# Optimization experiments

Measured on AMD Instinct MI355X. Metric: run time of the kernel, lower is better.

Reference implementation:

```python
import jax, jax.numpy as jnp
import numpy as np

N, E, DIM, H = 100000, 1600000, 128, 8
HD = DIM // H  # head_dim


def setup_inputs() -> dict:
    key = jax.random.key(0)
    ks = jax.random.split(key, 12)
    s = lambda k, sh, fan: jax.random.normal(k, sh, jnp.float32) * (1.0 / np.sqrt(fan))
    return {
        "x": jax.random.normal(ks[0], (N, DIM), jnp.float32),
        "src": jax.random.randint(ks[1], (E,), 0, N, jnp.int32),
        "dst": jax.random.randint(ks[2], (E,), 0, N, jnp.int32),
        # input_linear: dim -> dim
        "w_in": s(ks[3], (DIM, DIM), DIM), "b_in": jnp.zeros((DIM,), jnp.float32),
        # attn_linear_u: dim -> H (with bias); attn_linear_v: dim -> H (no bias)
        "w_au": s(ks[4], (DIM, H), DIM), "b_au": jnp.zeros((H,), jnp.float32),
        "w_av": s(ks[5], (DIM, H), DIM),
        # feed-forward: dim -> dim (hidden_dim_multiplier=1) -> dim
        "w1": s(ks[6], (DIM, DIM), DIM), "b1": jnp.zeros((DIM,), jnp.float32),
        "w2": s(ks[7], (DIM, DIM), DIM), "b2": jnpp if False else jnp.zeros((DIM,), jnp.float32),
    }


def reference(x, src, dst, w_in, b_in, w_au, b_au, w_av, w1, b1, w2, b2):
    n = x.shape[0]
    h = x @ w_in + b_in                      # [N, dim]
    a_u = h @ w_au + b_au                    # [N, H]
    a_v = h @ w_av                           # [N, H]
    # u_add_v: per-edge scores, then LeakyReLU(0.2)
    scores = jax.nn.leaky_relu(a_u[src] + a_v[dst], negative_slope=0.2)  # [E, H]
    # edge_softmax: normalize over incoming edges of each dst node
    smax = jax.ops.segment_max(scores, dst, num_segments=n)              # [N, H]
    ex = jnp.exp(scores - smax[dst])                                     # [E, H]
    denom = jax.ops.segment_sum(ex, dst, num_segments=n)                 # [N, H]
    probs = ex / denom[dst]                                              # [E, H]
    # u_mul_e_sum with x reshaped to [N, head_dim, H]
    hv = h.reshape(n, HD, H)
    msg = hv[src] * probs[:, None, :]                                    # [E, HD, H]
    agg = jax.ops.segment_sum(msg, dst, num_segments=n)                  # [N, HD, H]
    out = agg.reshape(n, DIM)
    # feed-forward (dropout=0, eval)
    out = jax.nn.gelu(out @ w1 + b1) @ w2 + b2
    return out
```

## Files before the change

kernel.cpp:

```cpp
#include <hip/hip_runtime.h>
#include <hip/hip_bf16.h>
#include <stdint.h>

#define DIM 128
#define NH 8
#define CH 4096
#define BK 128
#define LS 136
#define EBUF 4096

using bf16 = __hip_bfloat16;
typedef __attribute__((ext_vector_type(8))) short short8;
typedef __attribute__((ext_vector_type(4))) float floatx4;


__device__ inline float bf2f(unsigned short b) {
    return __uint_as_float(((unsigned)b) << 16);
}
__device__ inline unsigned short f2bf(float f) {
    unsigned u = __float_as_uint(f);
    u += 0x7FFFu + ((u >> 16) & 1u);
    return (unsigned short)(u >> 16);
}

__device__ inline float gelu_tanh(float x) {
    float x3 = x * x * x;
    float u = 0.7978845608028654f * (x + 0.044715f * x3);
    float e = __expf(2.f * u);
    float t = 1.f - 2.f / (e + 1.f);
    return 0.5f * x * (1.f + t);
}

__launch_bounds__(256)
__global__ void count_pre_kernel(const int* __restrict__ dst, int* __restrict__ mat,
                                 int E, int K, int B,
                                 const float* __restrict__ w_in, const float* __restrict__ w1,
                                 const float* __restrict__ w2, const float* __restrict__ w_au,
                                 const float* __restrict__ w_av,
                                 unsigned short* __restrict__ w_in_b, unsigned short* __restrict__ w1_b,
                                 unsigned short* __restrict__ w2_b, unsigned short* __restrict__ wc_b) {
    __shared__ int cnt[1024];
    const int b = blockIdx.x, tid = threadIdx.x;
    if (b < B) {
        for (int k = tid; k < K; k += 256) cnt[k] = 0;
        __syncthreads();
        const int base = b * CH, end = min(base + CH, E);
        for (int i = base + tid; i < end; i += 256)
            atomicAdd(&cnt[dst[i] >> 7], 1);
        __syncthreads();
        for (int k = tid; k < K; k += 256) mat[(size_t)k * B + b] = cnt[k];
    } else {
        int pb = b - B;
        if (pb < 12) {
            const int m = pb >> 2, qtr = pb & 3;
            const float* W = m == 0 ? w_in : (m == 1 ? w1 : w2);
            unsigned short* O = m == 0 ? w_in_b : (m == 1 ? w1_b : w2_b);
            const bool perm = (m == 1);
            #pragma unroll
            for (int i = 0; i < 16; ++i) {
                int o = qtr * 4096 + tid + i * 256;
                int k = o & 127, n = o >> 7;
                int krow = perm ? ((k & 15) * 8 + (k >> 4)) : k;
                O[o] = f2bf(W[krow * 128 + n]);
            }
        } else {
            #pragma unroll
            for (int i = 0; i < 8; ++i) {
                int o = tid + i * 256;
                int j = o >> 7, kt = o & 127;
                int ko = (kt & 15) * 8 + (kt >> 4);
                float v = (j < 8) ? w_au[ko * 8 + j] : w_av[ko * 8 + (j - 8)];
                wc_b[o] = f2bf(v);
            }
        }
    }
}

__device__ __forceinline__ void stage_pre(unsigned short* wt, const unsigned short* __restrict__ pre,
                                          int tid) {
    #pragma unroll
    for (int i = 0; i < 4; ++i) {
        int g = tid + i * 512;
        short8 v = *(const short8*)(pre + g * 8);
        *(short8*)(wt + (g >> 4) * LS + (g & 15) * 8) = v;
    }
}

__launch_bounds__(512)
__global__ void gemm_in_attn_kernel(const float* __restrict__ x, const unsigned short* __restrict__ w_in_b,
                                    const float* __restrict__ b_in,
                                    const unsigned short* __restrict__ wc_b, const float* __restrict__ b_au,
                                    bf16* __restrict__ h, float* __restrict__ au,
                                    float* __restrict__ av, int M) {
    __shared__ __align__(16) unsigned short wt[128 * LS];
    __shared__ __align__(16) unsigned short wc[16 * LS];
    const int tid = threadIdx.x;

    stage_pre(wt, w_in_b, tid);
    {
        int j = tid >> 5, kt4 = (tid & 31) * 4;
        const unsigned* s = (const unsigned*)(wc_b + j * 128 + kt4);
        unsigned* d = (unsigned*)(wc + j * LS + kt4);
        d[0] = s[0]; d[1] = s[1];
    }
    __syncthreads();

    const int wave = tid >> 6;
    const int lane = tid & 63;
    const int l15 = lane & 15;
    const int q = lane >> 4;
    const int rowbase = blockIdx.x * 128 + wave * 16;
    const int rowA = min(rowbase + l15, M - 1);

    floatx4 acc[8];
    #pragma unroll
    for (int c = 0; c < 8; ++c) acc[c] = (floatx4){0.f, 0.f, 0.f, 0.f};

    #pragma unroll
    for (int kk = 0; kk < 4; ++kk) {
        const float* ap = x + (size_t)rowA * 128 + kk * 32 + q * 8;
        floatx4 a0 = *(const floatx4*)ap;
        floatx4 a1 = *(const floatx4*)(ap + 4);
        union { short8 s; unsigned short u[8]; } cv;
        #pragma unroll
        for (int j = 0; j < 4; ++j) { cv.u[j] = f2bf(a0[j]); cv.u[4 + j] = f2bf(a1[j]); }
        short8 afrag = cv.s;
        #pragma unroll
        for (int c = 0; c < 8; ++c) {
            short8 bfrag = *(const short8*)(wt + (c * 16 + l15) * LS + kk * 32 + q * 8);
            acc[c] = __builtin_amdgcn_mfma_f32_16x16x32_bf16(afrag, bfrag, acc[c], 0, 0, 0);
        }
    }
    __syncthreads();

    const int rl0 = wave * 16 + q * 4;
    #pragma unroll
    for (int c = 0; c < 8; ++c) {
        int col = c * 16 + l15;
        int colw = (col & 7) * 16 + (col >> 3);
        float b = b_in[col];
        #pragma unroll
        for (int r = 0; r < 4; ++r)
            wt[(rl0 + r) * LS + colw] = f2bf(acc[c][r] + b);
    }
    __syncthreads();

    const int blk0 = blockIdx.x * 128;
    #pragma unroll
    for (int i = 0; i < 4; ++i) {
        int g = tid + i * 512;
        int row = g >> 4;
        if (blk0 + row < M) {
            short8 v = *(const short8*)(wt + row * LS + (g & 15) * 8);
            *(short8*)((unsigned short*)h + (size_t)(blk0 + row) * 128 + (g & 15) * 8) = v;
        }
    }

    floatx4 acc2 = (floatx4){0.f, 0.f, 0.f, 0.f};
    #pragma unroll
    for (int kk = 0; kk < 4; ++kk) {
        short8 af = *(const short8*)(wt + (wave * 16 + l15) * LS + kk * 32 + q * 8);
        short8 bf = *(const short8*)(wc + l15 * LS + kk * 32 + q * 8);
        acc2 = __builtin_amdgcn_mfma_f32_16x16x32_bf16(af, bf, acc2, 0, 0, 0);
    }
    {
        const int row0 = rowbase + q * 4;
        int col = l15;
        #pragma unroll
        for (int r = 0; r < 4; ++r) {
            int rr = row0 + r;
            if (rr < M) {
                if (col < 8) au[(size_t)rr * 8 + col] = acc2[r] + b_au[col];
                else         av[(size_t)rr * 8 + (col - 8)] = acc2[r];
            }
        }
    }
}

__launch_bounds__(512)
__global__ void ff_kernel(const bf16* __restrict__ A, const unsigned short* __restrict__ w1_b,
                          const float* __restrict__ b1, const unsigned short* __restrict__ w2_b,
                          const float* __restrict__ b2, float* __restrict__ out, int M) {
    __shared__ __align__(16) unsigned short wt[128 * LS];
    __shared__ __align__(16) unsigned short ht[128 * LS];
    const int tid = threadIdx.x;

    stage_pre(wt, w1_b, tid);
    __syncthreads();

    const int wave = tid >> 6;
    const int lane = tid & 63;
    const int l15 = lane & 15;
    const int q = lane >> 4;
    const int rowbase = blockIdx.x * 128 + wave * 16;
    const int rowA = min(rowbase + l15, M - 1);

    floatx4 acc[8];
    #pragma unroll
    for (int c = 0; c < 8; ++c) acc[c] = (floatx4){0.f, 0.f, 0.f, 0.f};

    #pragma unroll
    for (int kk = 0; kk < 4; ++kk) {
        short8 afrag = *(const short8*)((const unsigned short*)A + (size_t)rowA * 128 + kk * 32 + q * 8);
        #pragma unroll
        for (int c = 0; c < 8; ++c) {
            short8 bfrag = *(const short8*)(wt + (c * 16 + l15) * LS + kk * 32 + q * 8);
            acc[c] = __builtin_amdgcn_mfma_f32_16x16x32_bf16(afrag, bfrag, acc[c], 0, 0, 0);
        }
    }
    __syncthreads();

    stage_pre(wt, w2_b, tid);
    const int rl0 = wave * 16 + q * 4;
    #pragma unroll
    for (int c = 0; c < 8; ++c) {
        int col = c * 16 + l15;
        float b = b1[col];
        #pragma unroll
        for (int r = 0; r < 4; ++r)
            ht[(rl0 + r) * LS + col] = f2bf(gelu_tanh(acc[c][r] + b));
    }
    __syncthreads();

    floatx4 acc2[8];
    #pragma unroll
    for (int c = 0; c < 8; ++c) acc2[c] = (floatx4){0.f, 0.f, 0.f, 0.f};
    #pragma unroll
    for (int kk = 0; kk < 4; ++kk) {
        short8 af = *(const short8*)(ht + (wave * 16 + l15) * LS + kk * 32 + q * 8);
        #pragma unroll
        for (int c = 0; c < 8; ++c) {
            short8 bfrag = *(const short8*)(wt + (c * 16 + l15) * LS + kk * 32 + q * 8);
            acc2[c] = __builtin_amdgcn_mfma_f32_16x16x32_bf16(af, bfrag, acc2[c], 0, 0, 0);
        }
    }

    const int row0 = rowbase + q * 4;
    #pragma unroll
    for (int c = 0; c < 8; ++c) {
        int col = c * 16 + l15;
        float b = b2[col];
        #pragma unroll
        for (int r = 0; r < 4; ++r) {
            int rr = row0 + r;
            if (rr < M) out[(size_t)rr * 128 + col] = acc2[c][r] + b;
        }
    }
}


__launch_bounds__(64)
__global__ void scan_bucket_kernel(int* __restrict__ mat, int* __restrict__ btot, int B) {
    const int k = blockIdx.x;
    const int lane = threadIdx.x;
    const size_t base = (size_t)k * B;
    int carry = 0;
    for (int i0 = 0; i0 < B; i0 += 64) {
        int idx = i0 + lane;
        int v = (idx < B) ? mat[base + idx] : 0;
        int incl = v;
        #pragma unroll
        for (int off = 1; off < 64; off <<= 1) {
            int y = __shfl_up(incl, off);
            if (lane >= off) incl += y;
        }
        int tot = __shfl(incl, 63);
        if (idx < B) mat[base + idx] = carry + incl - v;
        carry += tot;
    }
    if (lane == 0) btot[k] = carry;
}

__launch_bounds__(64)
__global__ void scan_total_kernel(const int* __restrict__ btot, int* __restrict__ bbase, int K) {
    const int lane = threadIdx.x;
    int carry = 0;
    for (int i0 = 0; i0 < K; i0 += 64) {
        int idx = i0 + lane;
        int v = (idx < K) ? btot[idx] : 0;
        int incl = v;
        #pragma unroll
        for (int off = 1; off < 64; off <<= 1) {
            int y = __shfl_up(incl, off);
            if (lane >= off) incl += y;
        }
        int tot = __shfl(incl, 63);
        if (idx < K) bbase[idx] = carry + incl - v;
        carry += tot;
    }
}

__launch_bounds__(256)
__global__ void bucket_scatter_kernel(const int* __restrict__ src, const int* __restrict__ dst,
                                      int* __restrict__ lofs, unsigned* __restrict__ packed,
                                      int E, int K, int B) {
    __shared__ int hist[1024];
    __shared__ int cur[1024];
    __shared__ int wsum[4];
    const int b = blockIdx.x, tid = threadIdx.x;
    for (int k = tid; k < 1024; k += 256) hist[k] = 0;
    __syncthreads();
    const int base = b * CH, end = min(base + CH, E);
    for (int i = base + tid; i < end; i += 256)
        atomicAdd(&hist[dst[i] >> 7], 1);
    __syncthreads();
    int v[4]; int t = 0;
    #pragma unroll
    for (int j = 0; j < 4; ++j) { int x = hist[tid * 4 + j]; v[j] = t; t += x; }
    const int lane = tid & 63, wv = tid >> 6;
    int incl = t;
    #pragma unroll
    for (int off = 1; off < 64; off <<= 1) {
        int y = __shfl_up(incl, off);
        if (lane >= off) incl += y;
    }
    if (lane == 63) wsum[wv] = incl;
    __syncthreads();
    int woff = 0;
    #pragma unroll
    for (int w = 0; w < 4; ++w) if (w < wv) woff += wsum[w];
    int texcl = woff + incl - t;
    #pragma unroll
    for (int j = 0; j < 4; ++j) {
        int k = tid * 4 + j;
        int e = texcl + v[j];
        cur[k] = e;
        if (k < K) lofs[(size_t)b * K + k] = e;
    }
    __syncthreads();
    for (int i = base + tid; i < end; i += 256) {
        int d = dst[i], s = src[i];
        int pos = atomicAdd(&cur[d >> 7], 1);
        packed[(size_t)b * CH + pos] = (unsigned)s | ((unsigned)(d & 127) << 20);
    }
}

__launch_bounds__(256)
__global__ void bucket_csr_kernel(const unsigned* __restrict__ packed, const int* __restrict__ lofs,
                                  const int* __restrict__ mat,
                                  const int* __restrict__ bbase, const int* __restrict__ btot,
                                  int* __restrict__ rowptr, int* __restrict__ deg,
                                  int* __restrict__ esrc, int N, int E, int K, int B) {
    __shared__ unsigned ebuf[EBUF];
    __shared__ int hist[128], cur[128];
    __shared__ int wtot;
    const int k = blockIdx.x, tid = threadIdx.x;
    const int start = bbase[k];
    const int cnt = btot[k];

    for (int b = tid; b < B; b += 256) {
        int lo = lofs[(size_t)b * K + k];
        int chunk_len = min(CH, E - b * CH);
        int hi = (k + 1 < K) ? lofs[(size_t)b * K + k + 1] : chunk_len;
        int dbase = mat[(size_t)k * B + b];
        const unsigned* sp = packed + (size_t)b * CH;
        for (int j = lo; j < hi; ++j) ebuf[dbase + (j - lo)] = sp[j];
    }
    if (tid < 128) hist[tid] = 0;
    __syncthreads();

    for (int i = tid; i < cnt; i += 256)
        atomicAdd(&hist[ebuf[i] >> 20], 1);
    __syncthreads();

    const int lane = tid & 63;
    int v = (tid < 128) ? hist[tid] : 0;
    int incl = v;
    #pragma unroll
    for (int off = 1; off < 64; off <<= 1) {
        int y = __shfl_up(incl, off);
        if (lane >= off) incl += y;
    }
    if (tid == 63) wtot = incl;
    __syncthreads();
    int excl = incl - v + ((tid >= 64 && tid < 128) ? wtot : 0);
    if (tid < 128) {
        int n = k * BK + tid;
        if (n < N) { rowptr[n] = start + excl; deg[n] = v; }
        cur[tid] = excl;
    }
    __syncthreads();

    for (int i = tid; i < cnt; i += 256) {
        unsigned p = ebuf[i];
        int pos = atomicAdd(&cur[p >> 20], 1);
        esrc[start + pos] = (int)(p & 0xFFFFFu);
    }
}


__device__ __forceinline__ void unpack8fma(uint4 w, float p, float* o) {
    o[0] = fmaf(p, __uint_as_float(w.x << 16), o[0]);
    o[1] = fmaf(p, __uint_as_float(w.x & 0xFFFF0000u), o[1]);
    o[2] = fmaf(p, __uint_as_float(w.y << 16), o[2]);
    o[3] = fmaf(p, __uint_as_float(w.y & 0xFFFF0000u), o[3]);
    o[4] = fmaf(p, __uint_as_float(w.z << 16), o[4]);
    o[5] = fmaf(p, __uint_as_float(w.z & 0xFFFF0000u), o[5]);
    o[6] = fmaf(p, __uint_as_float(w.w << 16), o[6]);
    o[7] = fmaf(p, __uint_as_float(w.w & 0xFFFF0000u), o[7]);
}

template <bool MASKED>
__device__ __forceinline__ void do8e(const int* __restrict__ ep, int i, int nd,
                                     int e, int head, int d0b,
                                     const float* __restrict__ au,
                                     const char* __restrict__ hpb,
                                     float avh, float& l, float* o) {
    int idx = i + e;
    int s;
    float m = 1.f;
    if constexpr (MASKED) {
        s = ep[min(idx, nd - 1)];
        m = idx < nd ? 1.f : 0.f;
    } else {
        s = ep[idx];
    }
    float a = au[(s << 3) + head];
    size_t off = ((size_t)(unsigned)s) << 8;
    uint4 w0 = *(const uint4*)(hpb + off + d0b);
    uint4 w1 = *(const uint4*)(hpb + off + d0b + 16);
    float x = a + avh;
    x = fmaxf(x, 0.2f * x);
    float p = __expf(x);
    if constexpr (MASKED) p *= m;
    l += p;
    unpack8fma(w0, p, o);
    unpack8fma(w1, p, o + 8);
}

__launch_bounds__(256)
__global__ void agg_csr_kernel(const int* __restrict__ rowptr, const int* __restrict__ deg,
                               const int* __restrict__ esrc,
                               const float* __restrict__ au, const float* __restrict__ av,
                               const bf16* __restrict__ h, bf16* __restrict__ agg, int N) {
    const int node = (blockIdx.x * 256 + threadIdx.x) >> 6;
    if (node >= N) return;
    const int lane = threadIdx.x & 63;
    const int e = lane >> 3;
    const int head = lane & 7;
    const int d0b = head * 32;
    const char* hpb = (const char*)h;
    const int nd = deg[node];
    const int start = rowptr[node];
    const float avh = av[((size_t)node << 3) + head];
    const int* ep = esrc + start;

    float l0 = 0.f;
    float o[16];
    #pragma unroll
    for (int j = 0; j < 16; ++j) o[j] = 0.f;

    int i = 0;
    for (; i + 16 <= nd; i += 16) {
        do8e<false>(ep, i, nd, e, head, d0b, au, hpb, avh, l0, o);
        do8e<false>(ep, i + 8, nd, e, head, d0b, au, hpb, avh, l0, o);
    }
    if (i + 8 <= nd) { do8e<false>(ep, i, nd, e, head, d0b, au, hpb, avh, l0, o); i += 8; }
    if (i < nd) do8e<true>(ep, i, nd, e, head, d0b, au, hpb, avh, l0, o);

    #pragma unroll
    for (int j = 0; j < 16; ++j) {
        o[j] += __shfl_xor(o[j], 8);
        o[j] += __shfl_xor(o[j], 16);
        o[j] += __shfl_xor(o[j], 32);
    }
    l0 += __shfl_xor(l0, 8);
    l0 += __shfl_xor(l0, 16);
    l0 += __shfl_xor(l0, 32);

    if (lane < 8) {
        float inv = l0 > 0.f ? 1.f / l0 : 0.f;
        unsigned r[8];
        #pragma unroll
        for (int j = 0; j < 8; ++j)
            r[j] = ((unsigned)f2bf(o[2 * j + 1] * inv) << 16) | (unsigned)f2bf(o[2 * j] * inv);
        char* outp = (char*)agg + ((size_t)node << 8) + lane * 32;
        *(uint4*)outp = (uint4){r[0], r[1], r[2], r[3]};
        *(uint4*)(outp + 16) = (uint4){r[4], r[5], r[6], r[7]};
    }
}

extern "C" void kernel_launch(void* const* d_in, const int* in_sizes, int n_in,
                              void* d_out, int out_size, void* d_ws, size_t ws_size,
                              hipStream_t stream) {
    const float* x    = (const float*)d_in[0];
    const int*   src  = (const int*)d_in[1];
    const int*   dst  = (const int*)d_in[2];
    const float* w_in = (const float*)d_in[3];
    const float* b_in = (const float*)d_in[4];
    const float* w_au = (const float*)d_in[5];
    const float* b_au = (const float*)d_in[6];
    const float* w_av = (const float*)d_in[7];
    const float* w1   = (const float*)d_in[8];
    const float* b1   = (const float*)d_in[9];
    const float* w2   = (const float*)d_in[10];
    const float* b2   = (const float*)d_in[11];
    const int N = in_sizes[0] / DIM;
    const int E = in_sizes[1];
    const int K = (N + BK - 1) / BK;
    const int B = (E + CH - 1) / CH;

    char* p = (char*)d_ws;
    int*  deg    = (int*)p;  p += (size_t)N * 4;
    int*  rowptr = (int*)p;  p += (size_t)N * 4;
    int*  esrc   = (int*)p;  p += (size_t)E * 4;
    bf16* h      = (bf16*)p; p += (size_t)N * DIM * 2;
    float* au    = (float*)p; p += (size_t)N * NH * 4;
    float* av    = (float*)p; p += (size_t)N * NH * 4;
    unsigned short* w_in_b = (unsigned short*)p; p += 128 * 128 * 2;
    unsigned short* w1_b   = (unsigned short*)p; p += 128 * 128 * 2;
    unsigned short* w2_b   = (unsigned short*)p; p += 128 * 128 * 2;
    unsigned short* wc_b   = (unsigned short*)p; p += 16 * 128 * 2;
    bf16* agg    = (bf16*)p;  p += (size_t)N * DIM * 2;
    unsigned* packed = (unsigned*)agg;
    int* mat   = (int*)((char*)agg + (size_t)B * CH * 4);
    int* btot  = mat + (size_t)K * B;
    int* bbase = btot + K;
    int* lofs  = bbase + K;

    const int row_blocks = (N + 127) / 128;

    count_pre_kernel<<<B + 13, 256, 0, stream>>>(dst, mat, E, K, B,
                                                 w_in, w1, w2, w_au, w_av,
                                                 w_in_b, w1_b, w2_b, wc_b);

    gemm_in_attn_kernel<<<row_blocks, 512, 0, stream>>>(x, w_in_b, b_in, wc_b, b_au, h, au, av, N);

    scan_bucket_kernel<<<K, 64, 0, stream>>>(mat, btot, B);
    scan_total_kernel<<<1, 64, 0, stream>>>(btot, bbase, K);
    bucket_scatter_kernel<<<B, 256, 0, stream>>>(src, dst, lofs, packed, E, K, B);
    bucket_csr_kernel<<<K, 256, 0, stream>>>(packed, lofs, mat, bbase, btot,
                                             rowptr, deg, esrc, N, E, K, B);

    agg_csr_kernel<<<(N + 3) / 4, 256, 0, stream>>>(rowptr, deg, esrc, au, av, h, agg, N);

    ff_kernel<<<row_blocks, 512, 0, stream>>>(agg, w1_b, b1, w2_b, b2, (float*)d_out, N);
}
```

Before: 295.6 us.

## Fuse bucket count with scatter and fold bucket scans into GEMM launch

Per-chunk histogram counting and the bucket scatter now run in one kernel, so dst is read for the histogram only once instead of twice. The per-bucket scan over chunks moves into extra blocks of the input GEMM/attention kernel, and bucket base offsets come from an atomicAdd on a global counter. This replaces the single-block total scan and removes three kernel launches and their serialization. In exchange, bucket bases are assigned in nondeterministic order, and the scan assumes B is at most 512 chunks.

Measured after the change: 278.8 us. -5.7%, faster.

```diff
diff --git a/kernel.cpp b/kernel.cpp
--- a/kernel.cpp
+++ b/kernel.cpp
@@ -32,23 +32,58 @@
 }
 
 __launch_bounds__(256)
-__global__ void count_pre_kernel(const int* __restrict__ dst, int* __restrict__ mat,
-                                 int E, int K, int B,
-                                 const float* __restrict__ w_in, const float* __restrict__ w1,
-                                 const float* __restrict__ w2, const float* __restrict__ w_au,
-                                 const float* __restrict__ w_av,
-                                 unsigned short* __restrict__ w_in_b, unsigned short* __restrict__ w1_b,
-                                 unsigned short* __restrict__ w2_b, unsigned short* __restrict__ wc_b) {
-    __shared__ int cnt[1024];
+__global__ void scatter_pre_kernel(const int* __restrict__ src, const int* __restrict__ dst,
+                                   int* __restrict__ lofs, int* __restrict__ mat,
+                                   unsigned* __restrict__ packed, int* __restrict__ total,
+                                   int E, int K, int B,
+                                   const float* __restrict__ w_in, const float* __restrict__ w1,
+                                   const float* __restrict__ w2, const float* __restrict__ w_au,
+                                   const float* __restrict__ w_av,
+                                   unsigned short* __restrict__ w_in_b, unsigned short* __restrict__ w1_b,
+                                   unsigned short* __restrict__ w2_b, unsigned short* __restrict__ wc_b) {
+    __shared__ int hist[1024];
+    __shared__ int cur[1024];
+    __shared__ int wsum[4];
     const int b = blockIdx.x, tid = threadIdx.x;
     if (b < B) {
-        for (int k = tid; k < K; k += 256) cnt[k] = 0;
+        for (int k = tid; k < 1024; k += 256) hist[k] = 0;
         __syncthreads();
         const int base = b * CH, end = min(base + CH, E);
         for (int i = base + tid; i < end; i += 256)
-            atomicAdd(&cnt[dst[i] >> 7], 1);
+            atomicAdd(&hist[dst[i] >> 7], 1);
         __syncthreads();
-        for (int k = tid; k < K; k += 256) mat[(size_t)k * B + b] = cnt[k];
+        int v[4]; int t = 0;
+        #pragma unroll
+        for (int j = 0; j < 4; ++j) { int x = hist[tid * 4 + j]; v[j] = t; t += x; }
+        const int lane = tid & 63, wv = tid >> 6;
+        int incl = t;
+        #pragma unroll
+        for (int off = 1; off < 64; off <<= 1) {
+            int y = __shfl_up(incl, off);
+            if (lane >= off) incl += y;
+        }
+        if (lane == 63) wsum[wv] = incl;
+        __syncthreads();
+        int woff = 0;
+        #pragma unroll
+        for (int w = 0; w < 4; ++w) if (w < wv) woff += wsum[w];
+        int texcl = woff + incl - t;
+        #pragma unroll
+        for (int j = 0; j < 4; ++j) {
+            int k = tid * 4 + j;
+            int e = texcl + v[j];
+            cur[k] = e;
+            if (k < K) {
+                lofs[(size_t)b * K + k] = e;
+                mat[(size_t)b * 1024 + k] = hist[k];
+            }
+        }
+        __syncthreads();
+        for (int i = base + tid; i < end; i += 256) {
+            int d = dst[i], s = src[i];
+            int pos = atomicAdd(&cur[d >> 7], 1);
+            packed[(size_t)b * CH + pos] = (unsigned)s | ((unsigned)(d & 127) << 20);
+        }
     } else {
         int pb = b - B;
         if (pb < 12) {
@@ -72,6 +107,7 @@
                 float v = (j < 8) ? w_au[ko * 8 + j] : w_av[ko * 8 + (j - 8)];
                 wc_b[o] = f2bf(v);
             }
+            if (tid == 0) total[0] = 0;
         }
     }
 }
@@ -87,14 +123,38 @@
 }
 
 __launch_bounds__(512)
-__global__ void gemm_in_attn_kernel(const float* __restrict__ x, const unsigned short* __restrict__ w_in_b,
-                                    const float* __restrict__ b_in,
-                                    const unsigned short* __restrict__ wc_b, const float* __restrict__ b_au,
-                                    bf16* __restrict__ h, float* __restrict__ au,
-                                    float* __restrict__ av, int M) {
+__global__ void gia_scan_kernel(const float* __restrict__ x, const unsigned short* __restrict__ w_in_b,
+                                const float* __restrict__ b_in,
+                                const unsigned short* __restrict__ wc_b, const float* __restrict__ b_au,
+                                bf16* __restrict__ h, float* __restrict__ au,
+                                float* __restrict__ av, int M, int RB,
+                                const int* __restrict__ mat, int* __restrict__ matx,
+                                int* __restrict__ btot, int* __restrict__ bbase,
+                                int* __restrict__ total, int K, int B) {
     __shared__ __align__(16) unsigned short wt[128 * LS];
     __shared__ __align__(16) unsigned short wc[16 * LS];
+    __shared__ int sscr[8];
     const int tid = threadIdx.x;
+
+    if ((int)blockIdx.x >= RB) {
+        const int k = blockIdx.x - RB;
+        int v = (tid < B) ? mat[(size_t)tid * 1024 + k] : 0;
+        const int lane = tid & 63, wv = tid >> 6;
+        int incl = v;
+        #pragma unroll
+        for (int off = 1; off < 64; off <<= 1) {
+            int y = __shfl_up(incl, off);
+            if (lane >= off) incl += y;
+        }
+        if (lane == 63) sscr[wv] = incl;
+        __syncthreads();
+        int woff = 0, tot = 0;
+        #pragma unroll
+        for (int w = 0; w < 8; ++w) { int s = sscr[w]; if (w < wv) woff += s; tot += s; }
+        if (tid < B) matx[(size_t)k * B + tid] = woff + incl - v;
+        if (tid == 0) { bbase[k] = atomicAdd(total, tot); btot[k] = tot; }
+        return;
+    }
 
     stage_pre(wt, w_in_b, tid);
     {
@@ -248,96 +308,9 @@
     }
 }
 
-
-__launch_bounds__(64)
-__global__ void scan_bucket_kernel(int* __restrict__ mat, int* __restrict__ btot, int B) {
-    const int k = blockIdx.x;
-    const int lane = threadIdx.x;
-    const size_t base = (size_t)k * B;
-    int carry = 0;
-    for (int i0 = 0; i0 < B; i0 += 64) {
-        int idx = i0 + lane;
-        int v = (idx < B) ? mat[base + idx] : 0;
-        int incl = v;
-        #pragma unroll
-        for (int off = 1; off < 64; off <<= 1) {
-            int y = __shfl_up(incl, off);
-            if (lane >= off) incl += y;
-        }
-        int tot = __shfl(incl, 63);
-        if (idx < B) mat[base + idx] = carry + incl - v;
-        carry += tot;
-    }
-    if (lane == 0) btot[k] = carry;
-}
-
-__launch_bounds__(64)
-__global__ void scan_total_kernel(const int* __restrict__ btot, int* __restrict__ bbase, int K) {
-    const int lane = threadIdx.x;
-    int carry = 0;
-    for (int i0 = 0; i0 < K; i0 += 64) {
-        int idx = i0 + lane;
-        int v = (idx < K) ? btot[idx] : 0;
-        int incl = v;
-        #pragma unroll
-        for (int off = 1; off < 64; off <<= 1) {
-            int y = __shfl_up(incl, off);
-            if (lane >= off) incl += y;
-        }
-        int tot = __shfl(incl, 63);
-        if (idx < K) bbase[idx] = carry + incl - v;
-        carry += tot;
-    }
-}
-
-__launch_bounds__(256)
-__global__ void bucket_scatter_kernel(const int* __restrict__ src, const int* __restrict__ dst,
-                                      int* __restrict__ lofs, unsigned* __restrict__ packed,
-                                      int E, int K, int B) {
-    __shared__ int hist[1024];
-    __shared__ int cur[1024];
-    __shared__ int wsum[4];
-    const int b = blockIdx.x, tid = threadIdx.x;
-    for (int k = tid; k < 1024; k += 256) hist[k] = 0;
-    __syncthreads();
-    const int base = b * CH, end = min(base + CH, E);
-    for (int i = base + tid; i < end; i += 256)
-        atomicAdd(&hist[dst[i] >> 7], 1);
-    __syncthreads();
-    int v[4]; int t = 0;
-    #pragma unroll
-    for (int j = 0; j < 4; ++j) { int x = hist[tid * 4 + j]; v[j] = t; t += x; }
-    const int lane = tid & 63, wv = tid >> 6;
-    int incl = t;
-    #pragma unroll
-    for (int off = 1; off < 64; off <<= 1) {
-        int y = __shfl_up(incl, off);
-        if (lane >= off) incl += y;
-    }
-    if (lane == 63) wsum[wv] = incl;
-    __syncthreads();
-    int woff = 0;
-    #pragma unroll
-    for (int w = 0; w < 4; ++w) if (w < wv) woff += wsum[w];
-    int texcl = woff + incl - t;
-    #pragma unroll
-    for (int j = 0; j < 4; ++j) {
-        int k = tid * 4 + j;
-        int e = texcl + v[j];
-        cur[k] = e;
-        if (k < K) lofs[(size_t)b * K + k] = e;
-    }
-    __syncthreads();
-    for (int i = base + tid; i < end; i += 256) {
-        int d = dst[i], s = src[i];
-        int pos = atomicAdd(&cur[d >> 7], 1);
-        packed[(size_t)b * CH + pos] = (unsigned)s | ((unsigned)(d & 127) << 20);
-    }
-}
-
 __launch_bounds__(256)
 __global__ void bucket_csr_kernel(const unsigned* __restrict__ packed, const int* __restrict__ lofs,
-                                  const int* __restrict__ mat,
+                                  const int* __restrict__ matx,
                                   const int* __restrict__ bbase, const int* __restrict__ btot,
                                   int* __restrict__ rowptr, int* __restrict__ deg,
                                   int* __restrict__ esrc, int N, int E, int K, int B) {
@@ -352,7 +325,7 @@
         int lo = lofs[(size_t)b * K + k];
         int chunk_len = min(CH, E - b * CH);
         int hi = (k + 1 < K) ? lofs[(size_t)b * K + k + 1] : chunk_len;
-        int dbase = mat[(size_t)k * B + b];
+        int dbase = matx[(size_t)k * B + b];
         const unsigned* sp = packed + (size_t)b * CH;
         for (int j = lo; j < hi; ++j) ebuf[dbase + (j - lo)] = sp[j];
     }
@@ -511,25 +484,26 @@
     unsigned short* w1_b   = (unsigned short*)p; p += 128 * 128 * 2;
     unsigned short* w2_b   = (unsigned short*)p; p += 128 * 128 * 2;
     unsigned short* wc_b   = (unsigned short*)p; p += 16 * 128 * 2;
+    int* total = (int*)p; p += 64;
     bf16* agg    = (bf16*)p;  p += (size_t)N * DIM * 2;
     unsigned* packed = (unsigned*)agg;
     int* mat   = (int*)((char*)agg + (size_t)B * CH * 4);
-    int* btot  = mat + (size_t)K * B;
+    int* matx  = mat + (size_t)B * 1024;
+    int* btot  = matx + (size_t)K * B;
     int* bbase = btot + K;
     int* lofs  = bbase + K;
 
     const int row_blocks = (N + 127) / 128;
 
-    count_pre_kernel<<<B + 13, 256, 0, stream>>>(dst, mat, E, K, B,
-                                                 w_in, w1, w2, w_au, w_av,
-                                                 w_in_b, w1_b, w2_b, wc_b);
-
-    gemm_in_attn_kernel<<<row_blocks, 512, 0, stream>>>(x, w_in_b, b_in, wc_b, b_au, h, au, av, N);
-
-    scan_bucket_kernel<<<K, 64, 0, stream>>>(mat, btot, B);
-    scan_total_kernel<<<1, 64, 0, stream>>>(btot, bbase, K);
-    bucket_scatter_kernel<<<B, 256, 0, stream>>>(src, dst, lofs, packed, E, K, B);
-    bucket_csr_kernel<<<K, 256, 0, stream>>>(packed, lofs, mat, bbase, btot,
+    scatter_pre_kernel<<<B + 13, 256, 0, stream>>>(src, dst, lofs, mat, packed, total,
+                                                   E, K, B, w_in, w1, w2, w_au, w_av,
+                                                   w_in_b, w1_b, w2_b, wc_b);
+
+    gia_scan_kernel<<<row_blocks + K, 512, 0, stream>>>(x, w_in_b, b_in, wc_b, b_au,
+                                                        h, au, av, N, row_blocks,
+                                                        mat, matx, btot, bbase, total, K, B);
+
+    bucket_csr_kernel<<<K, 256, 0, stream>>>(packed, lofs, matx, bbase, btot,
                                              rowptr, deg, esrc, N, E, K, B);
 
     agg_csr_kernel<<<(N + 3) / 4, 256, 0, stream>>>(rowptr, deg, esrc, au, av, h, agg, N);
```
